# Optimization experiments

Hardware: AMD Instinct MI355X
Metric: run time of the kernel (lower is better)

Reference implementation:

```python
import jax, jax.numpy as jnp
import numpy as np

# static model config
V, N, L, E, H, KWIN, HOPS, NCLS = 50000, 128, 64, 300, 300, 40, 3, 6
KEFF = min(KWIN, N - 1)


def _gru_dir(x, mask, Wih, Whh, bih, bhh):
    # PyTorch GRU cell (gate order r,z,n). x: [T,B,D], mask: [T,B] bool.
    # Returns per-step outputs [T,B,H], zeroed at invalid steps (pad_packed behavior).
    h0 = jnp.zeros((x.shape[1], Whh.shape[1]), x.dtype)
    def step(h, xm):
        xt, mt = xm
        gi = xt @ Wih.T + bih
        gh = h @ Whh.T + bhh
        ir, iz, inn = jnp.split(gi, 3, axis=-1)
        hr, hz, hn = jnp.split(gh, 3, axis=-1)
        r = jax.nn.sigmoid(ir + hr)
        z = jax.nn.sigmoid(iz + hz)
        n = jnp.tanh(inn + r * hn)
        hnew = (1.0 - z) * n + z * h
        hnew = jnp.where(mt[:, None], hnew, h)
        return hnew, jnp.where(mt[:, None], hnew, 0.0)
    _, out = jax.lax.scan(step, h0, (x, mask))
    return out


def _bigru(x, lens, Wih, Whh, bih, bhh):
    # variable-length bidirectional GRU, equivalent to packed nn.GRU(bidirectional=True)
    T, B, _ = x.shape
    t = jnp.arange(T)[:, None]
    mask = t < lens[None, :]
    out_f = _gru_dir(x, mask, Wih[0], Whh[0], bih[0], bhh[0])
    ridx = jnp.clip(lens[None, :] - 1 - t, 0, T - 1)  # reverse-within-length index
    x_rev = jnp.take_along_axis(x, ridx[:, :, None], axis=0)
    out_rev = _gru_dir(x_rev, mask, Wih[1], Whh[1], bih[1], bhh[1])
    out_b = jnp.where(mask[:, :, None], jnp.take_along_axis(out_rev, ridx[:, :, None], axis=0), 0.0)
    return jnp.concatenate([out_f, out_b], axis=-1)


def _att_scan(inp, gates, Wr, br, Ur, bur, Ww, bw, Uw, bu):
    # AttnGRUCell loop: hi = g*tanh(W c + r*U h) + (1-g)*h, r = sigmoid(Wr c + Ur h)
    h0 = jnp.zeros((inp.shape[1], Ur.shape[1]), inp.dtype)
    def step(h, xg):
        x, g = xg
        r = jax.nn.sigmoid(x @ Wr.T + br + h @ Ur.T + bur)
        ht = jnp.tanh(x @ Ww.T + bw + r * (h @ Uw.T + bu))
        return g * ht + (1.0 - g) * h, None
    h, _ = jax.lax.scan(step, h0, (inp, gates))
    return h


def _forward(dialogue_ids, seq_lens, emb, utt_Wih, utt_Whh, utt_bih, utt_bhh, lin_w, lin_b, ctx_Wih, ctx_Whh, ctx_bih, ctx_bhh, att_Wr_w, att_Wr_b, att_Ur_w, att_Ur_b, att_W_w, att_W_b, att_U_w, att_U_b, cls_w, cls_b):
    x = emb[dialogue_ids].transpose(1, 0, 2)  # [L,N,E]
    utt_out = _bigru(x, seq_lens, utt_Wih, utt_Whh, utt_bih, utt_bhh)  # [L,N,2H]
    max_pool = jnp.max(utt_out, axis=0)  # [N,2H]; padded steps are 0 as in pad_packed
    u = jnp.tanh(max_pool @ lin_w.T + lin_b)  # [N,H] (dropout = identity, eval mode)
    # causal context windows: for query i (1..N-1) slot k holds u[i-KEFF+k], zero-padded
    i = jnp.arange(1, N)
    k = jnp.arange(KEFF)
    idx = i[:, None] - KEFF + k[None, :]  # [N-1,KEFF]
    valid = idx >= 0
    ctx = jnp.where(valid[:, :, None], u[jnp.clip(idx, 0)], 0.0)  # [N-1,KEFF,H]
    pad_mask = ~valid  # True at zero-padded slots -> masked in attention
    ctx_t = ctx.transpose(1, 0, 2)  # [KEFF,N-1,H]
    full = jnp.full((N - 1,), KEFF)
    mem_out = _bigru(ctx_t, full, ctx_Wih, ctx_Whh, ctx_bih, ctx_bhh)  # [KEFF,N-1,2H]
    mem_fwd, mem_bwd = jnp.split(mem_out, 2, axis=-1)
    mem_bank = (ctx_t + mem_fwd + mem_bwd).transpose(1, 0, 2)  # [N-1,KEFF,H]
    query = u[1:][:, None, :]  # [N-1,1,H]
    inp = mem_bank.transpose(1, 0, 2)  # [KEFF,N-1,H]
    for hop in range(HOPS):
        attn = jnp.einsum('bqh,bkh->bqk', query, mem_bank)  # [N-1,1,KEFF]
        attn = jnp.where(pad_mask[:, None, :], -1e10, attn)
        scores = jax.nn.softmax(attn, axis=-1)
        gates = scores.transpose(2, 0, 1)  # [KEFF,N-1,1]
        h_f = _att_scan(inp, gates, att_Wr_w[hop, 0], att_Wr_b[hop, 0], att_Ur_w[hop, 0], att_Ur_b[hop, 0], att_W_w[hop, 0], att_W_b[hop, 0], att_U_w[hop, 0], att_U_b[hop, 0])
        h_b = _att_scan(inp[::-1], gates[::-1], att_Wr_w[hop, 1], att_Wr_b[hop, 1], att_Ur_w[hop, 1], att_Ur_b[hop, 1], att_W_w[hop, 1], att_W_b[hop, 1], att_U_w[hop, 1], att_U_b[hop, 1])
        attn_out = jnp.concatenate([h_f, h_b], axis=-1)[:, None, :]  # [N-1,1,2H]
        a1, a2 = jnp.split(attn_out, 2, axis=-1)
        query = query + a1 + a2
    s_context = jnp.concatenate([u[:1][:, None, :], query], axis=0)[:, 0, :]  # [N,H]
    return s_context @ cls_w.T + cls_b  # [N,NCLS]


def setup_inputs() -> dict:
    ks = jax.random.split(jax.random.key(0), 32)
    def nrm(kk, shape):
        return jax.random.normal(kk, shape, jnp.float32) * 0.05
    inp = {}
    inp['dialogue_ids'] = jax.random.randint(ks[0], (N, L), 0, V)
    inp['seq_lens'] = jax.random.randint(ks[1], (N,), 1, L + 1)
    inp['emb'] = nrm(ks[2], (V, E))
    inp['utt_Wih'] = nrm(ks[3], (2, 3 * H, E))
    inp['utt_Whh'] = nrm(ks[4], (2, 3 * H, H))
    inp['utt_bih'] = nrm(ks[5], (2, 3 * H))
    inp['utt_bhh'] = nrm(ks[6], (2, 3 * H))
    inp['lin_w'] = nrm(ks[7], (H, 2 * H))
    inp['lin_b'] = nrm(ks[8], (H,))
    inp['ctx_Wih'] = nrm(ks[9], (2, 3 * H, H))
    inp['ctx_Whh'] = nrm(ks[10], (2, 3 * H, H))
    inp['ctx_bih'] = nrm(ks[11], (2, 3 * H))
    inp['ctx_bhh'] = nrm(ks[12], (2, 3 * H))
    inp['att_Wr_w'] = nrm(ks[13], (HOPS, 2, H, H))
    inp['att_Wr_b'] = nrm(ks[14], (HOPS, 2, H))
    inp['att_Ur_w'] = nrm(ks[15], (HOPS, 2, H, H))
    inp['att_Ur_b'] = nrm(ks[16], (HOPS, 2, H))
    inp['att_W_w'] = nrm(ks[17], (HOPS, 2, H, H))
    inp['att_W_b'] = nrm(ks[18], (HOPS, 2, H))
    inp['att_U_w'] = nrm(ks[19], (HOPS, 2, H, H))
    inp['att_U_b'] = nrm(ks[20], (HOPS, 2, H))
    inp['cls_w'] = nrm(ks[21], (NCLS, H))
    inp['cls_b'] = nrm(ks[22], (NCLS,))
    return inp


def reference(dialogue_ids, seq_lens, emb, utt_Wih, utt_Whh, utt_bih, utt_bhh, lin_w, lin_b, ctx_Wih, ctx_Whh, ctx_bih, ctx_bhh, att_Wr_w, att_Wr_b, att_Ur_w, att_Ur_b, att_W_w, att_W_b, att_U_w, att_U_b, cls_w, cls_b):
    return _forward(dialogue_ids, seq_lens, emb, utt_Wih, utt_Whh, utt_bih, utt_bhh, lin_w, lin_b, ctx_Wih, ctx_Whh, ctx_bih, ctx_bhh, att_Wr_w, att_Wr_b, att_Ur_w, att_Ur_b, att_W_w, att_W_b, att_U_w, att_U_b, cls_w, cls_b)
```

## Files before the change

kernel.cpp:

```cpp
#include <hip/hip_runtime.h>

static constexpr int NN   = 128;
static constexpr int LL   = 64;
static constexpr int KWIN = 40;
static constexpr int KEFF = 40;
static constexpr int NQ   = 127;
static constexpr int NCLS = 6;
static constexpr int KP   = 320;

static constexpr int GRU_RES = 10;
static constexpr int ATT_RES = 15;
static constexpr size_t GRU_LDS = (size_t)GRU_RES * 912 * 16 + (304 + 2700) * 4;
static constexpr size_t ATT_LDS = (size_t)ATT_RES * 608 * 16 + (320 + 1216 + 304 + 40 + 40) * 4;

typedef __attribute__((ext_vector_type(8))) short short8;
typedef __attribute__((ext_vector_type(4))) float floatx4;

__device__ __forceinline__ float sigm(float x) { return 1.f / (1.f + __expf(-x)); }
__device__ __forceinline__ short f2bf(float f) {
    unsigned x = __float_as_uint(f);
    unsigned r = (x + 0x7fffu + ((x >> 16) & 1u)) >> 16;
    return (short)r;
}
__device__ __forceinline__ void bfp(unsigned v, float& lo, float& hi) {
    lo = __uint_as_float(v << 16);
    hi = __uint_as_float(v & 0xffff0000u);
}
__device__ __forceinline__ void dot8(uint4 wv, float4 h0, float4 h1, float& acc) {
    float l0, u0, l1, u1, l2, u2, l3, u3;
    bfp(wv.x, l0, u0); bfp(wv.y, l1, u1);
    bfp(wv.z, l2, u2); bfp(wv.w, l3, u3);
    acc = fmaf(l0, h0.x, acc); acc = fmaf(u0, h0.y, acc);
    acc = fmaf(l1, h0.z, acc); acc = fmaf(u1, h0.w, acc);
    acc = fmaf(l2, h1.x, acc); acc = fmaf(u2, h1.y, acc);
    acc = fmaf(l3, h1.z, acc); acc = fmaf(u3, h1.w, acc);
}

__global__ void k_gather_bf16(const float* __restrict__ emb,
                              const int* __restrict__ ids,
                              short* __restrict__ A)
{
    int r = blockIdx.x;
    int n = r & (NN - 1);
    int t = r >> 7;
    int id = ids[n * LL + t];
    int e = threadIdx.x;
    float v = (e < 300) ? emb[(size_t)id * 300 + e] : 0.f;
    A[(size_t)r * KP + e] = f2bf(v);
}

__global__ void k_conv4(const float* __restrict__ s0, const float* __restrict__ s1,
                        const float* __restrict__ s2, const float* __restrict__ s3,
                        short* __restrict__ d0, short* __restrict__ d1,
                        short* __restrict__ d2, short* __restrict__ d3)
{
    int which = blockIdx.y;
    const float* s = (which == 0) ? s0 : (which == 1) ? s1 : (which == 2) ? s2 : s3;
    short* d = (which == 0) ? d0 : (which == 1) ? d1 : (which == 2) ? d2 : d3;
    int r = blockIdx.x, e = threadIdx.x;
    float v = (e < 300) ? s[(size_t)r * 300 + e] : 0.f;
    d[(size_t)r * KP + e] = f2bf(v);
}

__global__ void k_pack_gru2(const float* __restrict__ W0, const float* __restrict__ W1,
                            short* __restrict__ d0, short* __restrict__ d1)
{
    const float* W = blockIdx.y ? W1 : W0;
    short* dst = blockIdx.y ? d1 : d0;
    int idx = blockIdx.x * 256 + threadIdx.x;
    if (idx >= 2 * 39 * 900) return;
    int u = idx % 900, dc = idx / 900;
    int c = dc % 39, d = dc / 39;
    int cs = c / 3, s = c - cs * 3;
    int p = u / 300, m = u - p * 300;
    const float* src = W + ((size_t)d * 900 + s * 300 + m) * 300 + p * 100;
    short8 sv;
#pragma unroll
    for (int i = 0; i < 8; ++i) {
        int cl = cs * 8 + i;
        sv[i] = (cl < 100) ? f2bf(src[cl]) : (short)0;
    }
    *(short8*)(dst + ((size_t)(d * 39 + c) * 912 + u) * 8) = sv;
}

__global__ void k_pack_att(const float* __restrict__ Ur, const float* __restrict__ Uw,
                           short* __restrict__ dst)
{
    int idx = blockIdx.x * 256 + threadIdx.x;
    if (idx >= 6 * 40 * 600) return;
    int u = idx % 600, hc = idx / 600;
    int c = hc % 40, hd = hc / 40;
    int cs = c >> 1, s = c & 1;
    int p = u / 300, m = u - p * 300;
    int lim = p ? 140 : 160;
    const float* src = (s ? Uw : Ur) + ((size_t)hd * 300 + m) * 300 + 160 * p;
    short8 sv;
#pragma unroll
    for (int i = 0; i < 8; ++i) {
        int cl = cs * 8 + i;
        sv[i] = (cl < lim) ? f2bf(src[cl]) : (short)0;
    }
    *(short8*)(dst + ((size_t)(hd * 40 + c) * 608 + u) * 8) = sv;
}

__global__ __launch_bounds__(256)
void k_mgemm(const short* __restrict__ A, const short* __restrict__ B,
             const float* __restrict__ bias, float* __restrict__ C,
             int R, int Cc)
{
    __shared__ short As[128 * 40];
    __shared__ short Bs[128 * 40];
    const int tid = threadIdx.x;
    const int r0 = blockIdx.y * 128, c0 = blockIdx.x * 128;
    const int w = tid >> 6, lane = tid & 63;
    const int m16 = lane & 15, quad = lane >> 4;
    const int wm = w & 1, wn = w >> 1;
    floatx4 acc[4][4];
#pragma unroll
    for (int i = 0; i < 4; ++i)
#pragma unroll
        for (int j = 0; j < 4; ++j) acc[i][j] = (floatx4){0.f, 0.f, 0.f, 0.f};

    const int ra0 = tid >> 2,         sa0 = tid & 3;
    const int ra1 = (tid + 256) >> 2, sa1 = tid & 3;
    const short8 za = {0,0,0,0,0,0,0,0};
    short8 na0 = za, na1 = za, nb0 = za, nb1 = za;
    if (r0 + ra0 < R)  na0 = *(const short8*)(A + (size_t)(r0 + ra0) * KP + sa0 * 8);
    if (r0 + ra1 < R)  na1 = *(const short8*)(A + (size_t)(r0 + ra1) * KP + sa1 * 8);
    if (c0 + ra0 < Cc) nb0 = *(const short8*)(B + (size_t)(c0 + ra0) * KP + sa0 * 8);
    if (c0 + ra1 < Cc) nb1 = *(const short8*)(B + (size_t)(c0 + ra1) * KP + sa1 * 8);

#pragma unroll
    for (int it = 0; it < KP / 32; ++it) {
        *(short8*)(As + ra0 * 40 + sa0 * 8) = na0;
        *(short8*)(As + ra1 * 40 + sa1 * 8) = na1;
        *(short8*)(Bs + ra0 * 40 + sa0 * 8) = nb0;
        *(short8*)(Bs + ra1 * 40 + sa1 * 8) = nb1;
        __syncthreads();
        if (it + 1 < KP / 32) {
            const int k0 = (it + 1) * 32;
            na0 = za; na1 = za; nb0 = za; nb1 = za;
            if (r0 + ra0 < R)  na0 = *(const short8*)(A + (size_t)(r0 + ra0) * KP + k0 + sa0 * 8);
            if (r0 + ra1 < R)  na1 = *(const short8*)(A + (size_t)(r0 + ra1) * KP + k0 + sa1 * 8);
            if (c0 + ra0 < Cc) nb0 = *(const short8*)(B + (size_t)(c0 + ra0) * KP + k0 + sa0 * 8);
            if (c0 + ra1 < Cc) nb1 = *(const short8*)(B + (size_t)(c0 + ra1) * KP + k0 + sa1 * 8);
        }
        short8 af[4], bfr[4];
#pragma unroll
        for (int mt = 0; mt < 4; ++mt)
            af[mt] = *(const short8*)(As + (wm * 64 + mt * 16 + m16) * 40 + quad * 8);
#pragma unroll
        for (int nt = 0; nt < 4; ++nt)
            bfr[nt] = *(const short8*)(Bs + (wn * 64 + nt * 16 + m16) * 40 + quad * 8);
#pragma unroll
        for (int mt = 0; mt < 4; ++mt)
#pragma unroll
            for (int nt = 0; nt < 4; ++nt)
                acc[mt][nt] = __builtin_amdgcn_mfma_f32_16x16x32_bf16(
                    af[mt], bfr[nt], acc[mt][nt], 0, 0, 0);
        __syncthreads();
    }
#pragma unroll
    for (int mt = 0; mt < 4; ++mt) {
#pragma unroll
        for (int nt = 0; nt < 4; ++nt) {
            int col = c0 + wn * 64 + nt * 16 + m16;
            if (col >= Cc) continue;
            float bv = bias ? bias[col] : 0.f;
#pragma unroll
            for (int i = 0; i < 4; ++i) {
                int row = r0 + wm * 64 + mt * 16 + quad * 4 + i;
                if (row < R) C[(size_t)row * Cc + col] = acc[mt][nt][i] + bv;
            }
        }
    }
}

__global__ __launch_bounds__(256)
void k_gemm(const float* __restrict__ A, const float* __restrict__ B,
            const float* __restrict__ bias, float* __restrict__ C,
            int R, int Cc, int K, int actTanh)
{
    __shared__ __align__(16) float Asm[16][132];
    __shared__ __align__(16) float Bsm[16][132];
    const int tid = threadIdx.x;
    const int r0 = blockIdx.y * 128, c0 = blockIdx.x * 128;
    const int li = tid >> 1, lk = (tid & 1) * 8;
    const int tx = tid & 15, ty = tid >> 4;
    float acc[8][8];
#pragma unroll
    for (int i = 0; i < 8; ++i)
#pragma unroll
        for (int j = 0; j < 8; ++j) acc[i][j] = 0.f;
    const int nch = (K + 15) >> 4;
    for (int ch = 0; ch < nch; ++ch) {
        const int k0 = ch * 16;
        {
            float v[8];
            int gr = r0 + li, kb = k0 + lk;
            if (gr < R && kb + 8 <= K) {
                const float* p = A + (size_t)gr * K + kb;
                *(float4*)&v[0] = *(const float4*)p;
                *(float4*)&v[4] = *(const float4*)(p + 4);
            } else {
#pragma unroll
                for (int z = 0; z < 8; ++z) {
                    int k = kb + z;
                    v[z] = (gr < R && k < K) ? A[(size_t)gr * K + k] : 0.f;
                }
            }
#pragma unroll
            for (int z = 0; z < 8; ++z) Asm[lk + z][li] = v[z];
        }
        {
            float v[8];
            int gr = c0 + li, kb = k0 + lk;
            if (gr < Cc && kb + 8 <= K) {
                const float* p = B + (size_t)gr * K + kb;
                *(float4*)&v[0] = *(const float4*)p;
                *(float4*)&v[4] = *(const float4*)(p + 4);
            } else {
#pragma unroll
                for (int z = 0; z < 8; ++z) {
                    int k = kb + z;
                    v[z] = (gr < Cc && k < K) ? B[(size_t)gr * K + k] : 0.f;
                }
            }
#pragma unroll
            for (int z = 0; z < 8; ++z) Bsm[lk + z][li] = v[z];
        }
        __syncthreads();
#pragma unroll
        for (int kk = 0; kk < 16; ++kk) {
            float a[8], b[8];
            *(float4*)&a[0] = *(const float4*)&Asm[kk][ty * 8];
            *(float4*)&a[4] = *(const float4*)&Asm[kk][ty * 8 + 4];
            *(float4*)&b[0] = *(const float4*)&Bsm[kk][tx * 8];
            *(float4*)&b[4] = *(const float4*)&Bsm[kk][tx * 8 + 4];
#pragma unroll
            for (int i = 0; i < 8; ++i)
#pragma unroll
                for (int j = 0; j < 8; ++j) acc[i][j] = fmaf(a[i], b[j], acc[i][j]);
        }
        __syncthreads();
    }
#pragma unroll
    for (int i = 0; i < 8; ++i) {
        int r = r0 + ty * 8 + i;
        if (r >= R) continue;
#pragma unroll
        for (int j = 0; j < 8; ++j) {
            int c = c0 + tx * 8 + j;
            if (c >= Cc) continue;
            float v = acc[i][j];
            if (bias) v += bias[c];
            if (actTanh) v = tanhf(v);
            C[(size_t)r * Cc + c] = v;
        }
    }
}

template<bool IS_UTT>
__device__ __forceinline__ void gru_scan_body(
    const short* __restrict__ Wp,
    const float* __restrict__ bhh,
    const float* __restrict__ gi,
    int d, int chain, int NB, int len,
    float* __restrict__ outp)
{
    extern __shared__ char smem[];
    short* wlds = (short*)smem;
    float* hs   = (float*)(smem + (size_t)GRU_RES * 912 * 16);
    float* pds  = hs + 304;
    const int tid = threadIdx.x;
    const int p = tid / 300, m = tid - p * 300;
    const uint4* wall = (const uint4*)(Wp + (size_t)d * 39 * 912 * 8);
    if (tid < 912) {
#pragma unroll
        for (int c = 0; c < GRU_RES; ++c)
            *(uint4*)(wlds + ((size_t)c * 912 + tid) * 8) = wall[(size_t)c * 912 + tid];
    }
    if (tid < 304) hs[tid] = 0.f;
    float br = 0.f, bz = 0.f, bn = 0.f;
    if (tid < 300) {
        br = bhh[d * 900 + tid];
        bz = bhh[d * 900 + 300 + tid];
        bn = bhh[d * 900 + 600 + tid];
    }
    float mx = -1e30f;
    __syncthreads();
    for (int t = 0; t < len; ++t) {
        int ts = d ? (len - 1 - t) : t;
        float g0 = 0.f, g1 = 0.f, g2 = 0.f;
        if (tid < 300) {
            size_t row = ((size_t)(ts * NB + chain)) * 1800 + d * 900 + tid;
            g0 = gi[row]; g1 = gi[row + 300]; g2 = gi[row + 600];
        }
        if (tid < 900) {
            const int hb = 100 * p;
            float a0 = 0.f, a1 = 0.f, a2 = 0.f;
            uint4 ring[6];
#pragma unroll
            for (int i = 0; i < 6; ++i) ring[i] = wall[(size_t)(GRU_RES + i) * 912 + tid];
#pragma unroll
            for (int c = 0; c < GRU_RES; ++c) {
                int cs = c / 3, s = c - 3 * cs;
                float4 h0 = *(const float4*)&hs[hb + 8 * cs];
                float4 h1 = *(const float4*)&hs[hb + 8 * cs + 4];
                uint4 wv = *(const uint4*)(wlds + ((size_t)c * 912 + tid) * 8);
                if (s == 0) dot8(wv, h0, h1, a0);
                else if (s == 1) dot8(wv, h0, h1, a1);
                else dot8(wv, h0, h1, a2);
            }
#pragma unroll
            for (int i = 0; i < 39 - GRU_RES; ++i) {
                int c = GRU_RES + i, cs = c / 3, s = c - 3 * cs;
                uint4 wv = ring[i % 6];
                if (i + 6 < 39 - GRU_RES)
                    ring[i % 6] = wall[(size_t)(c + 6) * 912 + tid];
                float4 h0 = *(const float4*)&hs[hb + 8 * cs];
                float4 h1 = *(const float4*)&hs[hb + 8 * cs + 4];
                if (s == 0) dot8(wv, h0, h1, a0);
                else if (s == 1) dot8(wv, h0, h1, a1);
                else dot8(wv, h0, h1, a2);
            }
            pds[(0 * 3 + p) * 300 + m] = a0;
            pds[(1 * 3 + p) * 300 + m] = a1;
            pds[(2 * 3 + p) * 300 + m] = a2;
        }
        __syncthreads();
        if (tid < 300) {
            float dr = pds[tid] + pds[300 + tid] + pds[600 + tid] + br;
            float dz = pds[900 + tid] + pds[1200 + tid] + pds[1500 + tid] + bz;
            float dn = pds[1800 + tid] + pds[2100 + tid] + pds[2400 + tid] + bn;
            float r = sigm(g0 + dr);
            float z = sigm(g1 + dz);
            float nv = tanhf(g2 + r * dn);
            float hv = (1.f - z) * nv + z * hs[tid];
            hs[tid] = hv;
            if (IS_UTT) mx = fmaxf(mx, hv);
            else outp[(size_t)ts * 300 + tid] = hv;
        }
        __syncthreads();
    }
    if (IS_UTT && tid < 300) {
        if (len < LL) mx = fmaxf(mx, 0.f);
        outp[tid] = mx;
    }
}

__global__ __launch_bounds__(960, 1)
void k_utt_scan(const short* __restrict__ Wp, const float* __restrict__ bhh,
                const float* __restrict__ gi, const int* __restrict__ lens,
                float* __restrict__ maxpool)
{
    const int d = blockIdx.y, n = blockIdx.x;
    gru_scan_body<true>(Wp, bhh, gi, d, n, NN, lens[n],
                        maxpool + (size_t)n * 600 + d * 300);
}

__global__ __launch_bounds__(960, 1)
void k_ctx_scan(const short* __restrict__ Wp, const float* __restrict__ bhh,
                const float* __restrict__ gi, float* __restrict__ hout)
{
    const int d = blockIdx.y, q = blockIdx.x;
    gru_scan_body<false>(Wp, bhh, gi, d, q, NQ, KEFF,
                         hout + (((size_t)d * NQ + q) * KEFF) * 300);
}

__global__ void k_build_ctxA(const float* __restrict__ u, short* __restrict__ Actx,
                             float* __restrict__ query)
{
    int rkq = blockIdx.x;
    int k = rkq / NQ, q = rkq - k * NQ;
    int src = q + 1 - KWIN + k;
    int e = threadIdx.x;
    float v = (e < 300 && src >= 0) ? u[(size_t)src * 300 + e] : 0.f;
    Actx[(size_t)rkq * KP + e] = f2bf(v);
    if (k == 0 && e < 300)
        query[(size_t)q * 300 + e] = u[(size_t)(q + 1) * 300 + e];
}

__global__ void k_combine(const float* __restrict__ u, const float* __restrict__ hout,
                          float* __restrict__ mem_bank, short* __restrict__ mrkq)
{
    int rkq = blockIdx.x;
    int k = rkq / NQ, q = rkq - k * NQ;
    int src = q + 1 - KWIN + k;
    int e = threadIdx.x;
    float v = 0.f;
    if (e < 300) {
        float c = (src >= 0) ? u[(size_t)src * 300 + e] : 0.f;
        v = c + hout[((size_t)q * KEFF + k) * 300 + e]
              + hout[(((size_t)NQ + q) * KEFF + k) * 300 + e];
        mem_bank[((size_t)q * KEFF + k) * 300 + e] = v;
    }
    mrkq[(size_t)rkq * KP + e] = f2bf(v);
}

__global__ __launch_bounds__(640, 1)
void k_att_scan(const short* __restrict__ Wp,
                const float* __restrict__ burb,
                const float* __restrict__ bub,
                const float* __restrict__ xgr,
                const float* __restrict__ xgw,
                const float* __restrict__ query,
                const float* __restrict__ membank,
                float* __restrict__ hbuf,
                int hop)
{
    extern __shared__ char smem[];
    short* wlds  = (short*)smem;
    float* hs    = (float*)(smem + (size_t)ATT_RES * 608 * 16);
    float* pds   = hs + 320;
    float* qv    = pds + 1216;
    float* gates = qv + 304;
    float* scr   = gates + 40;
    const int d = blockIdx.y, q = blockIdx.x, tid = threadIdx.x;
    const int hd = hop * 2 + d;
    const int p = tid / 300, m = tid - p * 300;
    const uint4* wall = (const uint4*)(Wp + (size_t)hd * 40 * 608 * 8);
    if (tid < 608) {
#pragma unroll
        for (int c = 0; c < ATT_RES; ++c)
            *(uint4*)(wlds + ((size_t)c * 608 + tid) * 8) = wall[(size_t)c * 608 + tid];
    }
    if (tid < 320) {
        hs[tid] = 0.f;
        qv[tid] = (tid < 300) ? query[(size_t)q * 300 + tid] : 0.f;
    }
    float bur = 0.f, bu = 0.f;
    if (tid < 300) { bur = burb[hd * 300 + tid]; bu = bub[hd * 300 + tid]; }
    __syncthreads();
    if (tid < 320) {
        int k = tid >> 3, part = tid & 7;
        const float* mrow = membank + ((size_t)q * KEFF + k) * 300;
        int e0 = part * 38, e1 = e0 + 38 > 300 ? 300 : e0 + 38;
        float acc = 0.f;
        for (int e = e0; e < e1; ++e) acc = fmaf(qv[e], mrow[e], acc);
        acc += __shfl_xor(acc, 1);
        acc += __shfl_xor(acc, 2);
        acc += __shfl_xor(acc, 4);
        if (part == 0) scr[k] = acc;
    }
    __syncthreads();
    if (tid < 64) {
        float s = (tid < KEFF) ? scr[tid] : -1e30f;
        if (tid < KWIN - 1 - q) s = -1e10f;
        float mxs = s;
        for (int o = 32; o > 0; o >>= 1) mxs = fmaxf(mxs, __shfl_xor(mxs, o));
        float e = (tid < KEFF) ? __expf(s - mxs) : 0.f;
        float sm = e;
        for (int o = 32; o > 0; o >>= 1) sm += __shfl_xor(sm, o);
        if (tid < KEFF) gates[tid] = e / sm;
    }
    __syncthreads();
    for (int t = 0; t < KEFF; ++t) {
        int kq = d ? (KEFF - 1 - t) : t;
        float xr = 0.f, xw = 0.f, gt = 0.f;
        if (tid < 300) {
            size_t xi = ((size_t)(kq * NQ + q)) * 1800 + (size_t)hd * 300 + tid;
            xr = xgr[xi]; xw = xgw[xi];
            gt = gates[kq];
        }
        if (tid < 600) {
            const int hb = 160 * p;
            float a0 = 0.f, a1 = 0.f;
            uint4 ring[6];
#pragma unroll
            for (int i = 0; i < 6; ++i) ring[i] = wall[(size_t)(ATT_RES + i) * 608 + tid];
#pragma unroll
            for (int c = 0; c < ATT_RES; ++c) {
                int cs = c >> 1, s = c & 1;
                float4 h0 = *(const float4*)&hs[hb + 8 * cs];
                float4 h1 = *(const float4*)&hs[hb + 8 * cs + 4];
                uint4 wv = *(const uint4*)(wlds + ((size_t)c * 608 + tid) * 8);
                if (s == 0) dot8(wv, h0, h1, a0);
                else dot8(wv, h0, h1, a1);
            }
#pragma unroll
            for (int i = 0; i < 40 - ATT_RES; ++i) {
                int c = ATT_RES + i, cs = c >> 1, s = c & 1;
                uint4 wv = ring[i % 6];
                if (i + 6 < 40 - ATT_RES)
                    ring[i % 6] = wall[(size_t)(c + 6) * 608 + tid];
                float4 h0 = *(const float4*)&hs[hb + 8 * cs];
                float4 h1 = *(const float4*)&hs[hb + 8 * cs + 4];
                if (s == 0) dot8(wv, h0, h1, a0);
                else dot8(wv, h0, h1, a1);
            }
            pds[(0 * 2 + p) * 304 + m] = a0;
            pds[(1 * 2 + p) * 304 + m] = a1;
        }
        __syncthreads();
        if (tid < 300) {
            float dr = pds[tid] + pds[304 + tid] + bur;
            float dw = pds[608 + tid] + pds[912 + tid] + bu;
            float r = sigm(xr + dr);
            float ht = tanhf(xw + r * dw);
            hs[tid] = gt * ht + (1.f - gt) * hs[tid];
        }
        __syncthreads();
    }
    if (tid < 300)
        hbuf[((size_t)d * NQ + q) * 300 + tid] = hs[tid];
}

__global__ void k_qupd(float* __restrict__ query, const float* __restrict__ hbuf)
{
    int q = blockIdx.x;
    for (int e = threadIdx.x; e < 300; e += blockDim.x)
        query[(size_t)q * 300 + e] += hbuf[(size_t)q * 300 + e]
                                    + hbuf[(size_t)(NQ + q) * 300 + e];
}

__global__ __launch_bounds__(64)
void k_cls(const float* __restrict__ u, const float* __restrict__ query,
           const float* __restrict__ cw, const float* __restrict__ cb,
           float* __restrict__ out)
{
    int n = blockIdx.x;
    const float* srow = (n == 0) ? u : (query + (size_t)(n - 1) * 300);
    int c = threadIdx.x & 7;
    int part = threadIdx.x >> 3;
    float p = 0.f;
    if (c < NCLS) {
        for (int e = part; e < 300; e += 8) p = fmaf(srow[e], cw[c * 300 + e], p);
    }
    p += __shfl_xor(p, 8);
    p += __shfl_xor(p, 16);
    p += __shfl_xor(p, 32);
    if (part == 0 && c < NCLS) out[n * NCLS + c] = p + cb[c];
}

extern "C" void kernel_launch(void* const* d_in, const int* in_sizes, int n_in,
                              void* d_out, int out_size, void* d_ws, size_t ws_size,
                              hipStream_t stream)
{
    const int* ids  = (const int*)d_in[0];
    const int* lens = (const int*)d_in[1];
    const float* emb   = (const float*)d_in[2];
    const float* uWih  = (const float*)d_in[3];
    const float* uWhh  = (const float*)d_in[4];
    const float* ubih  = (const float*)d_in[5];
    const float* ubhh  = (const float*)d_in[6];
    const float* linw  = (const float*)d_in[7];
    const float* linb  = (const float*)d_in[8];
    const float* cWih  = (const float*)d_in[9];
    const float* cWhh  = (const float*)d_in[10];
    const float* cbih  = (const float*)d_in[11];
    const float* cbhh  = (const float*)d_in[12];
    const float* aWr_w = (const float*)d_in[13];
    const float* aWr_b = (const float*)d_in[14];
    const float* aUr_w = (const float*)d_in[15];
    const float* aUr_b = (const float*)d_in[16];
    const float* aW_w  = (const float*)d_in[17];
    const float* aW_b  = (const float*)d_in[18];
    const float* aU_w  = (const float*)d_in[19];
    const float* aU_b  = (const float*)d_in[20];
    const float* clsw  = (const float*)d_in[21];
    const float* clsb  = (const float*)d_in[22];
    float* out = (float*)d_out;
    (void)in_sizes; (void)n_in; (void)out_size; (void)ws_size;

    (void)hipFuncSetAttribute((const void*)k_utt_scan,
            hipFuncAttributeMaxDynamicSharedMemorySize, (int)GRU_LDS);
    (void)hipFuncSetAttribute((const void*)k_ctx_scan,
            hipFuncAttributeMaxDynamicSharedMemorySize, (int)GRU_LDS);
    (void)hipFuncSetAttribute((const void*)k_att_scan,
            hipFuncAttributeMaxDynamicSharedMemorySize, (int)ATT_LDS);

    char* base = (char*)d_ws;
    size_t off = 0;
    auto alloc = [&](size_t b) -> void* {
        void* r = (void*)(base + off);
        off += (b + 255) & ~(size_t)255;
        return r;
    };
    short* A_utt  = (short*)alloc((size_t)8192 * KP * 2);
    float* giU    = (float*)alloc((size_t)8192 * 1800 * 4);
    float* giC    = (float*)alloc((size_t)5080 * 1800 * 4);
    short* wUihB  = (short*)alloc((size_t)1800 * KP * 2);
    short* wCihB  = (short*)alloc((size_t)1800 * KP * 2);
    short* wArB   = (short*)alloc((size_t)1800 * KP * 2);
    short* wAwB   = (short*)alloc((size_t)1800 * KP * 2);
    short* wPackU = (short*)alloc((size_t)2 * 39 * 912 * 8 * 2);
    short* wPackC = (short*)alloc((size_t)2 * 39 * 912 * 8 * 2);
    short* wPackA = (short*)alloc((size_t)6 * 40 * 608 * 8 * 2);
    short* Actx   = (short*)alloc((size_t)5080 * KP * 2);
    float* hout   = (float*)alloc((size_t)2 * NQ * KEFF * 300 * 4);
    float* membank= (float*)alloc((size_t)NQ * KEFF * 300 * 4);
    short* mrkq   = (short*)alloc((size_t)5080 * KP * 2);
    float* mpool  = (float*)alloc((size_t)NN * 600 * 4);
    float* uu     = (float*)alloc((size_t)NN * 300 * 4);
    float* query  = (float*)alloc((size_t)NQ * 300 * 4);
    float* hbuf   = (float*)alloc((size_t)2 * NQ * 300 * 4);
    float* xgr = giU;
    float* xgw = giC;

    const int RKQ = NQ * KEFF;

    k_conv4<<<dim3(1800, 4), dim3(320), 0, stream>>>(uWih, cWih, aWr_w, aW_w,
                                                     wUihB, wCihB, wArB, wAwB);
    k_pack_gru2<<<dim3((2 * 39 * 900 + 255) / 256, 2), dim3(256), 0, stream>>>(
        uWhh, cWhh, wPackU, wPackC);
    k_pack_att<<<dim3((6 * 40 * 600 + 255) / 256), dim3(256), 0, stream>>>(aUr_w, aU_w, wPackA);

    k_gather_bf16<<<dim3(LL * NN), dim3(320), 0, stream>>>(emb, ids, A_utt);
    k_mgemm<<<dim3(15, 64), dim3(256), 0, stream>>>(A_utt, wUihB, ubih, giU, 8192, 1800);
    k_utt_scan<<<dim3(NN, 2), dim3(960), GRU_LDS, stream>>>(wPackU, ubhh, giU, lens, mpool);
    k_gemm<<<dim3(3, 1), dim3(256), 0, stream>>>(mpool, linw, linb, uu, NN, 300, 600, 1);
    k_build_ctxA<<<dim3(RKQ), dim3(320), 0, stream>>>(uu, Actx, query);
    k_mgemm<<<dim3(15, 40), dim3(256), 0, stream>>>(Actx, wCihB, cbih, giC, RKQ, 1800);
    k_ctx_scan<<<dim3(NQ, 2), dim3(960), GRU_LDS, stream>>>(wPackC, cbhh, giC, hout);
    k_combine<<<dim3(RKQ), dim3(320), 0, stream>>>(uu, hout, membank, mrkq);
    k_mgemm<<<dim3(15, 40), dim3(256), 0, stream>>>(mrkq, wArB, aWr_b, xgr, RKQ, 1800);
    k_mgemm<<<dim3(15, 40), dim3(256), 0, stream>>>(mrkq, wAwB, aW_b, xgw, RKQ, 1800);
    for (int hop = 0; hop < 3; ++hop) {
        k_att_scan<<<dim3(NQ, 2), dim3(640), ATT_LDS, stream>>>(
            wPackA, aUr_b, aU_b, xgr, xgw, query, membank, hbuf, hop);
        k_qupd<<<dim3(NQ), dim3(128), 0, stream>>>(query, hbuf);
    }
    k_cls<<<dim3(NN), dim3(64), 0, stream>>>(uu, query, clsw, clsb, out);
}
```

Before: 1.297 ms.

## Fuse gathers into GEMM loads, store gate projections as bf16, drop query-update kernels

```diff
diff --git a/kernel.cpp b/kernel.cpp
--- a/kernel.cpp
+++ b/kernel.cpp
@@ -9,7 +9,7 @@
 static constexpr int KP   = 320;
 
 static constexpr int GRU_RES = 10;
-static constexpr int ATT_RES = 15;
+static constexpr int ATT_RES = 16;
 static constexpr size_t GRU_LDS = (size_t)GRU_RES * 912 * 16 + (304 + 2700) * 4;
 static constexpr size_t ATT_LDS = (size_t)ATT_RES * 608 * 16 + (320 + 1216 + 304 + 40 + 40) * 4;
 
@@ -21,6 +21,9 @@
     unsigned x = __float_as_uint(f);
     unsigned r = (x + 0x7fffu + ((x >> 16) & 1u)) >> 16;
     return (short)r;
+}
+__device__ __forceinline__ float b2f(short u) {
+    return __uint_as_float(((unsigned)(unsigned short)u) << 16);
 }
 __device__ __forceinline__ void bfp(unsigned v, float& lo, float& hi) {
     lo = __uint_as_float(v << 16);
@@ -34,19 +37,6 @@
     acc = fmaf(l1, h0.z, acc); acc = fmaf(u1, h0.w, acc);
     acc = fmaf(l2, h1.x, acc); acc = fmaf(u2, h1.y, acc);
     acc = fmaf(l3, h1.z, acc); acc = fmaf(u3, h1.w, acc);
-}
-
-__global__ void k_gather_bf16(const float* __restrict__ emb,
-                              const int* __restrict__ ids,
-                              short* __restrict__ A)
-{
-    int r = blockIdx.x;
-    int n = r & (NN - 1);
-    int t = r >> 7;
-    int id = ids[n * LL + t];
-    int e = threadIdx.x;
-    float v = (e < 300) ? emb[(size_t)id * 300 + e] : 0.f;
-    A[(size_t)r * KP + e] = f2bf(v);
 }
 
 __global__ void k_conv4(const float* __restrict__ s0, const float* __restrict__ s1,
@@ -103,11 +93,56 @@
     *(short8*)(dst + ((size_t)(hd * 40 + c) * 608 + u) * 8) = sv;
 }
 
+template<int MODE>
+__device__ __forceinline__ short8 load_a8(const short* __restrict__ Abf,
+                                          const float* __restrict__ emb,
+                                          const int* __restrict__ ids,
+                                          const float* __restrict__ uu,
+                                          int row, int R, int o)
+{
+    short8 z = {0,0,0,0,0,0,0,0};
+    if (MODE == 0) {
+        if (row < R) return *(const short8*)(Abf + (size_t)row * KP + o);
+        return z;
+    }
+    const float* src;
+    if (MODE == 1) {
+        int n = row & (NN - 1), t = row >> 7;
+        src = emb + (size_t)ids[n * LL + t] * 300;
+    } else {
+        if (row >= R) return z;
+        int k = row / NQ, q = row - k * NQ;
+        int s = q + 1 - KWIN + k;
+        if (s < 0) return z;
+        src = uu + (size_t)s * 300;
+    }
+    short8 r = z;
+    if (o + 8 <= 300) {
+        float4 f0 = *(const float4*)(src + o);
+        float4 f1 = *(const float4*)(src + o + 4);
+        r[0] = f2bf(f0.x); r[1] = f2bf(f0.y); r[2] = f2bf(f0.z); r[3] = f2bf(f0.w);
+        r[4] = f2bf(f1.x); r[5] = f2bf(f1.y); r[6] = f2bf(f1.z); r[7] = f2bf(f1.w);
+    } else if (o < 300) {
+#pragma unroll
+        for (int i = 0; i < 8; ++i)
+            r[i] = (o + i < 300) ? f2bf(src[o + i]) : (short)0;
+    }
+    return r;
+}
+
+template<int MODE>
 __global__ __launch_bounds__(256)
-void k_mgemm(const short* __restrict__ A, const short* __restrict__ B,
-             const float* __restrict__ bias, float* __restrict__ C,
+void k_mgemm(const short* __restrict__ Abf, const float* __restrict__ emb,
+             const int* __restrict__ ids, const float* __restrict__ uu,
+             const short* __restrict__ B, const float* __restrict__ bias,
+             short* __restrict__ C,
+             const short* __restrict__ B2, const float* __restrict__ bias2,
+             short* __restrict__ C2,
              int R, int Cc)
 {
+    const short* Bp = blockIdx.z ? B2 : B;
+    const float* bp = blockIdx.z ? bias2 : bias;
+    short* Cp = blockIdx.z ? C2 : C;
     __shared__ short As[128 * 40];
     __shared__ short Bs[128 * 40];
     const int tid = threadIdx.x;
@@ -124,11 +159,11 @@
     const int ra0 = tid >> 2,         sa0 = tid & 3;
     const int ra1 = (tid + 256) >> 2, sa1 = tid & 3;
     const short8 za = {0,0,0,0,0,0,0,0};
-    short8 na0 = za, na1 = za, nb0 = za, nb1 = za;
-    if (r0 + ra0 < R)  na0 = *(const short8*)(A + (size_t)(r0 + ra0) * KP + sa0 * 8);
-    if (r0 + ra1 < R)  na1 = *(const short8*)(A + (size_t)(r0 + ra1) * KP + sa1 * 8);
-    if (c0 + ra0 < Cc) nb0 = *(const short8*)(B + (size_t)(c0 + ra0) * KP + sa0 * 8);
-    if (c0 + ra1 < Cc) nb1 = *(const short8*)(B + (size_t)(c0 + ra1) * KP + sa1 * 8);
+    short8 na0, na1, nb0 = za, nb1 = za;
+    na0 = load_a8<MODE>(Abf, emb, ids, uu, r0 + ra0, R, sa0 * 8);
+    na1 = load_a8<MODE>(Abf, emb, ids, uu, r0 + ra1, R, sa1 * 8);
+    if (c0 + ra0 < Cc) nb0 = *(const short8*)(Bp + (size_t)(c0 + ra0) * KP + sa0 * 8);
+    if (c0 + ra1 < Cc) nb1 = *(const short8*)(Bp + (size_t)(c0 + ra1) * KP + sa1 * 8);
 
 #pragma unroll
     for (int it = 0; it < KP / 32; ++it) {
@@ -139,11 +174,11 @@
         __syncthreads();
         if (it + 1 < KP / 32) {
             const int k0 = (it + 1) * 32;
-            na0 = za; na1 = za; nb0 = za; nb1 = za;
-            if (r0 + ra0 < R)  na0 = *(const short8*)(A + (size_t)(r0 + ra0) * KP + k0 + sa0 * 8);
-            if (r0 + ra1 < R)  na1 = *(const short8*)(A + (size_t)(r0 + ra1) * KP + k0 + sa1 * 8);
-            if (c0 + ra0 < Cc) nb0 = *(const short8*)(B + (size_t)(c0 + ra0) * KP + k0 + sa0 * 8);
-            if (c0 + ra1 < Cc) nb1 = *(const short8*)(B + (size_t)(c0 + ra1) * KP + k0 + sa1 * 8);
+            na0 = load_a8<MODE>(Abf, emb, ids, uu, r0 + ra0, R, k0 + sa0 * 8);
+            na1 = load_a8<MODE>(Abf, emb, ids, uu, r0 + ra1, R, k0 + sa1 * 8);
+            nb0 = za; nb1 = za;
+            if (c0 + ra0 < Cc) nb0 = *(const short8*)(Bp + (size_t)(c0 + ra0) * KP + k0 + sa0 * 8);
+            if (c0 + ra1 < Cc) nb1 = *(const short8*)(Bp + (size_t)(c0 + ra1) * KP + k0 + sa1 * 8);
         }
         short8 af[4], bfr[4];
 #pragma unroll
@@ -166,11 +201,11 @@
         for (int nt = 0; nt < 4; ++nt) {
             int col = c0 + wn * 64 + nt * 16 + m16;
             if (col >= Cc) continue;
-            float bv = bias ? bias[col] : 0.f;
+            float bv = bp ? bp[col] : 0.f;
 #pragma unroll
             for (int i = 0; i < 4; ++i) {
                 int row = r0 + wm * 64 + mt * 16 + quad * 4 + i;
-                if (row < R) C[(size_t)row * Cc + col] = acc[mt][nt][i] + bv;
+                if (row < R) Cp[(size_t)row * Cc + col] = f2bf(acc[mt][nt][i] + bv);
             }
         }
     }
@@ -264,7 +299,7 @@
 __device__ __forceinline__ void gru_scan_body(
     const short* __restrict__ Wp,
     const float* __restrict__ bhh,
-    const float* __restrict__ gi,
+    const short* __restrict__ gi,
     int d, int chain, int NB, int len,
     float* __restrict__ outp)
 {
@@ -294,14 +329,14 @@
         float g0 = 0.f, g1 = 0.f, g2 = 0.f;
         if (tid < 300) {
             size_t row = ((size_t)(ts * NB + chain)) * 1800 + d * 900 + tid;
-            g0 = gi[row]; g1 = gi[row + 300]; g2 = gi[row + 600];
+            g0 = b2f(gi[row]); g1 = b2f(gi[row + 300]); g2 = b2f(gi[row + 600]);
         }
         if (tid < 900) {
             const int hb = 100 * p;
             float a0 = 0.f, a1 = 0.f, a2 = 0.f;
-            uint4 ring[6];
-#pragma unroll
-            for (int i = 0; i < 6; ++i) ring[i] = wall[(size_t)(GRU_RES + i) * 912 + tid];
+            uint4 ring[8];
+#pragma unroll
+            for (int i = 0; i < 8; ++i) ring[i] = wall[(size_t)(GRU_RES + i) * 912 + tid];
 #pragma unroll
             for (int c = 0; c < GRU_RES; ++c) {
                 int cs = c / 3, s = c - 3 * cs;
@@ -315,9 +350,9 @@
 #pragma unroll
             for (int i = 0; i < 39 - GRU_RES; ++i) {
                 int c = GRU_RES + i, cs = c / 3, s = c - 3 * cs;
-                uint4 wv = ring[i % 6];
-                if (i + 6 < 39 - GRU_RES)
-                    ring[i % 6] = wall[(size_t)(c + 6) * 912 + tid];
+                uint4 wv = ring[i & 7];
+                if (i + 8 < 39 - GRU_RES)
+                    ring[i & 7] = wall[(size_t)(c + 8) * 912 + tid];
                 float4 h0 = *(const float4*)&hs[hb + 8 * cs];
                 float4 h1 = *(const float4*)&hs[hb + 8 * cs + 4];
                 if (s == 0) dot8(wv, h0, h1, a0);
@@ -351,7 +386,7 @@
 
 __global__ __launch_bounds__(960, 1)
 void k_utt_scan(const short* __restrict__ Wp, const float* __restrict__ bhh,
-                const float* __restrict__ gi, const int* __restrict__ lens,
+                const short* __restrict__ gi, const int* __restrict__ lens,
                 float* __restrict__ maxpool)
 {
     const int d = blockIdx.y, n = blockIdx.x;
@@ -361,28 +396,16 @@
 
 __global__ __launch_bounds__(960, 1)
 void k_ctx_scan(const short* __restrict__ Wp, const float* __restrict__ bhh,
-                const float* __restrict__ gi, float* __restrict__ hout)
+                const short* __restrict__ gi, float* __restrict__ hout)
 {
     const int d = blockIdx.y, q = blockIdx.x;
     gru_scan_body<false>(Wp, bhh, gi, d, q, NQ, KEFF,
                          hout + (((size_t)d * NQ + q) * KEFF) * 300);
 }
 
-__global__ void k_build_ctxA(const float* __restrict__ u, short* __restrict__ Actx,
-                             float* __restrict__ query)
-{
-    int rkq = blockIdx.x;
-    int k = rkq / NQ, q = rkq - k * NQ;
-    int src = q + 1 - KWIN + k;
-    int e = threadIdx.x;
-    float v = (e < 300 && src >= 0) ? u[(size_t)src * 300 + e] : 0.f;
-    Actx[(size_t)rkq * KP + e] = f2bf(v);
-    if (k == 0 && e < 300)
-        query[(size_t)q * 300 + e] = u[(size_t)(q + 1) * 300 + e];
-}
-
 __global__ void k_combine(const float* __restrict__ u, const float* __restrict__ hout,
-                          float* __restrict__ mem_bank, short* __restrict__ mrkq)
+                          float* __restrict__ mem_bank, short* __restrict__ mrkq,
+                          float* __restrict__ query0)
 {
     int rkq = blockIdx.x;
     int k = rkq / NQ, q = rkq - k * NQ;
@@ -394,6 +417,7 @@
         v = c + hout[((size_t)q * KEFF + k) * 300 + e]
               + hout[(((size_t)NQ + q) * KEFF + k) * 300 + e];
         mem_bank[((size_t)q * KEFF + k) * 300 + e] = v;
+        if (k == 0) query0[(size_t)q * 300 + e] = u[(size_t)(q + 1) * 300 + e];
     }
     mrkq[(size_t)rkq * KP + e] = f2bf(v);
 }
@@ -402,9 +426,9 @@
 void k_att_scan(const short* __restrict__ Wp,
                 const float* __restrict__ burb,
                 const float* __restrict__ bub,
-                const float* __restrict__ xgr,
-                const float* __restrict__ xgw,
-                const float* __restrict__ query,
+                const short* __restrict__ xgr,
+                const short* __restrict__ xgw,
+                const float* __restrict__ query0,
                 const float* __restrict__ membank,
                 float* __restrict__ hbuf,
                 int hop)
@@ -427,7 +451,14 @@
     }
     if (tid < 320) {
         hs[tid] = 0.f;
-        qv[tid] = (tid < 300) ? query[(size_t)q * 300 + tid] : 0.f;
+        float qq = 0.f;
+        if (tid < 300) {
+            qq = query0[(size_t)q * 300 + tid];
+            for (int j = 0; j < hop; ++j)
+                qq += hbuf[((size_t)(2 * j) * NQ + q) * 300 + tid]
+                    + hbuf[((size_t)(2 * j + 1) * NQ + q) * 300 + tid];
+        }
+        qv[tid] = qq;
     }
     float bur = 0.f, bu = 0.f;
     if (tid < 300) { bur = burb[hd * 300 + tid]; bu = bub[hd * 300 + tid]; }
@@ -460,15 +491,15 @@
         float xr = 0.f, xw = 0.f, gt = 0.f;
         if (tid < 300) {
             size_t xi = ((size_t)(kq * NQ + q)) * 1800 + (size_t)hd * 300 + tid;
-            xr = xgr[xi]; xw = xgw[xi];
+            xr = b2f(xgr[xi]); xw = b2f(xgw[xi]);
             gt = gates[kq];
         }
         if (tid < 600) {
             const int hb = 160 * p;
             float a0 = 0.f, a1 = 0.f;
-            uint4 ring[6];
-#pragma unroll
-            for (int i = 0; i < 6; ++i) ring[i] = wall[(size_t)(ATT_RES + i) * 608 + tid];
+            uint4 ring[8];
+#pragma unroll
+            for (int i = 0; i < 8; ++i) ring[i] = wall[(size_t)(ATT_RES + i) * 608 + tid];
 #pragma unroll
             for (int c = 0; c < ATT_RES; ++c) {
                 int cs = c >> 1, s = c & 1;
@@ -481,9 +512,9 @@
 #pragma unroll
             for (int i = 0; i < 40 - ATT_RES; ++i) {
                 int c = ATT_RES + i, cs = c >> 1, s = c & 1;
-                uint4 wv = ring[i % 6];
-                if (i + 6 < 40 - ATT_RES)
-                    ring[i % 6] = wall[(size_t)(c + 6) * 608 + tid];
+                uint4 wv = ring[i & 7];
+                if (i + 8 < 40 - ATT_RES)
+                    ring[i & 7] = wall[(size_t)(c + 8) * 608 + tid];
                 float4 h0 = *(const float4*)&hs[hb + 8 * cs];
                 float4 h1 = *(const float4*)&hs[hb + 8 * cs + 4];
                 if (s == 0) dot8(wv, h0, h1, a0);
@@ -503,29 +534,32 @@
         __syncthreads();
     }
     if (tid < 300)
-        hbuf[((size_t)d * NQ + q) * 300 + tid] = hs[tid];
-}
-
-__global__ void k_qupd(float* __restrict__ query, const float* __restrict__ hbuf)
-{
-    int q = blockIdx.x;
-    for (int e = threadIdx.x; e < 300; e += blockDim.x)
-        query[(size_t)q * 300 + e] += hbuf[(size_t)q * 300 + e]
-                                    + hbuf[(size_t)(NQ + q) * 300 + e];
+        hbuf[((size_t)hd * NQ + q) * 300 + tid] = hs[tid];
 }
 
 __global__ __launch_bounds__(64)
-void k_cls(const float* __restrict__ u, const float* __restrict__ query,
+void k_cls(const float* __restrict__ u, const float* __restrict__ query0,
+           const float* __restrict__ hbuf,
            const float* __restrict__ cw, const float* __restrict__ cb,
            float* __restrict__ out)
 {
     int n = blockIdx.x;
-    const float* srow = (n == 0) ? u : (query + (size_t)(n - 1) * 300);
     int c = threadIdx.x & 7;
     int part = threadIdx.x >> 3;
     float p = 0.f;
     if (c < NCLS) {
-        for (int e = part; e < 300; e += 8) p = fmaf(srow[e], cw[c * 300 + e], p);
+        for (int e = part; e < 300; e += 8) {
+            float s;
+            if (n == 0) s = u[e];
+            else {
+                int q = n - 1;
+                s = query0[(size_t)q * 300 + e];
+#pragma unroll
+                for (int j = 0; j < 6; ++j)
+                    s += hbuf[((size_t)j * NQ + q) * 300 + e];
+            }
+            p = fmaf(s, cw[c * 300 + e], p);
+        }
     }
     p += __shfl_xor(p, 8);
     p += __shfl_xor(p, 16);
@@ -577,9 +611,8 @@
         off += (b + 255) & ~(size_t)255;
         return r;
     };
-    short* A_utt  = (short*)alloc((size_t)8192 * KP * 2);
-    float* giU    = (float*)alloc((size_t)8192 * 1800 * 4);
-    float* giC    = (float*)alloc((size_t)5080 * 1800 * 4);
+    short* giU    = (short*)alloc((size_t)8192 * 1800 * 2);
+    short* giC    = (short*)alloc((size_t)5080 * 1800 * 2);
     short* wUihB  = (short*)alloc((size_t)1800 * KP * 2);
     short* wCihB  = (short*)alloc((size_t)1800 * KP * 2);
     short* wArB   = (short*)alloc((size_t)1800 * KP * 2);
@@ -587,16 +620,15 @@
     short* wPackU = (short*)alloc((size_t)2 * 39 * 912 * 8 * 2);
     short* wPackC = (short*)alloc((size_t)2 * 39 * 912 * 8 * 2);
     short* wPackA = (short*)alloc((size_t)6 * 40 * 608 * 8 * 2);
-    short* Actx   = (short*)alloc((size_t)5080 * KP * 2);
     float* hout   = (float*)alloc((size_t)2 * NQ * KEFF * 300 * 4);
     float* membank= (float*)alloc((size_t)NQ * KEFF * 300 * 4);
     short* mrkq   = (short*)alloc((size_t)5080 * KP * 2);
     float* mpool  = (float*)alloc((size_t)NN * 600 * 4);
     float* uu     = (float*)alloc((size_t)NN * 300 * 4);
-    float* query  = (float*)alloc((size_t)NQ * 300 * 4);
-    float* hbuf   = (float*)alloc((size_t)2 * NQ * 300 * 4);
-    float* xgr = giU;
-    float* xgw = giC;
+    float* query0 = (float*)alloc((size_t)NQ * 300 * 4);
+    float* hbuf   = (float*)alloc((size_t)6 * NQ * 300 * 4);
+    short* xgr = giU;
+    short* xgw = giC;
 
     const int RKQ = NQ * KEFF;
 
@@ -606,20 +638,22 @@
         uWhh, cWhh, wPackU, wPackC);
     k_pack_att<<<dim3((6 * 40 * 600 + 255) / 256), dim3(256), 0, stream>>>(aUr_w, aU_w, wPackA);
 
-    k_gather_bf16<<<dim3(LL * NN), dim3(320), 0, stream>>>(emb, ids, A_utt);
-    k_mgemm<<<dim3(15, 64), dim3(256), 0, stream>>>(A_utt, wUihB, ubih, giU, 8192, 1800);
+    k_mgemm<1><<<dim3(15, 64, 1), dim3(256), 0, stream>>>(
+        nullptr, emb, ids, nullptr, wUihB, ubih, giU,
+        wUihB, ubih, giU, 8192, 1800);
     k_utt_scan<<<dim3(NN, 2), dim3(960), GRU_LDS, stream>>>(wPackU, ubhh, giU, lens, mpool);
     k_gemm<<<dim3(3, 1), dim3(256), 0, stream>>>(mpool, linw, linb, uu, NN, 300, 600, 1);
-    k_build_ctxA<<<dim3(RKQ), dim3(320), 0, stream>>>(uu, Actx, query);
-    k_mgemm<<<dim3(15, 40), dim3(256), 0, stream>>>(Actx, wCihB, cbih, giC, RKQ, 1800);
+    k_mgemm<2><<<dim3(15, 40, 1), dim3(256), 0, stream>>>(
+        nullptr, nullptr, nullptr, uu, wCihB, cbih, giC,
+        wCihB, cbih, giC, RKQ, 1800);
     k_ctx_scan<<<dim3(NQ, 2), dim3(960), GRU_LDS, stream>>>(wPackC, cbhh, giC, hout);
-    k_combine<<<dim3(RKQ), dim3(320), 0, stream>>>(uu, hout, membank, mrkq);
-    k_mgemm<<<dim3(15, 40), dim3(256), 0, stream>>>(mrkq, wArB, aWr_b, xgr, RKQ, 1800);
-    k_mgemm<<<dim3(15, 40), dim3(256), 0, stream>>>(mrkq, wAwB, aW_b, xgw, RKQ, 1800);
+    k_combine<<<dim3(RKQ), dim3(320), 0, stream>>>(uu, hout, membank, mrkq, query0);
+    k_mgemm<0><<<dim3(15, 40, 2), dim3(256), 0, stream>>>(
+        mrkq, nullptr, nullptr, nullptr, wArB, aWr_b, xgr,
+        wAwB, aW_b, xgw, RKQ, 1800);
     for (int hop = 0; hop < 3; ++hop) {
         k_att_scan<<<dim3(NQ, 2), dim3(640), ATT_LDS, stream>>>(
-            wPackA, aUr_b, aU_b, xgr, xgw, query, membank, hbuf, hop);
-        k_qupd<<<dim3(NQ), dim3(128), 0, stream>>>(query, hbuf);
-    }
-    k_cls<<<dim3(NN), dim3(64), 0, stream>>>(uu, query, clsw, clsb, out);
-}
+            wPackA, aUr_b, aU_b, xgr, xgw, query0, membank, hbuf, hop);
+    }
+    k_cls<<<dim3(NN), dim3(64), 0, stream>>>(uu, query0, hbuf, clsw, clsb, out);
+}
```

Result: no change. 1.310 ms (+1.1%).
